# Optimization experiments

Hardware: AMD Instinct MI355X
Metric: run time of the kernel (lower is better)

## Reference

```python
import jax, jax.numpy as jnp
import numpy as np

N, H, n = 256, 64, 32
EPS = 1e-8  # eigenvalue floor for sqrt/rsqrt/log (SPD by construction, guard fp32)


def _sym_apply(X, fn, clip=True):
    """Apply scalar function fn to the eigenvalues of symmetric X (batched)."""
    w, V = jnp.linalg.eigh(X)
    if clip:
        w = jnp.clip(w, EPS)
    return jnp.einsum('...ij,...j,...kj->...ik', V, fn(w), V)


def _barygeom(Xf):
    """Riemannian barycenter via one Karcher-flow step (m_fun.BaryGeom, k=1).
    Xf: (M, n, n) SPD batch -> (n, n) Frechet mean."""
    G = jnp.mean(Xf, axis=0)                                   # arithmetic init
    G_sq = _sym_apply(G, jnp.sqrt)                             # G^{1/2}
    G_isq = _sym_apply(G, lambda w: 1.0 / jnp.sqrt(w))         # G^{-1/2}
    # mean of log(G^{-1/2} X G^{-1/2}) over the batch
    L = jnp.mean(_sym_apply(G_isq @ Xf @ G_isq, jnp.log), axis=0)
    expL = _sym_apply(L, jnp.exp, clip=False)                  # L symmetric, not PSD
    return G_sq @ expL @ G_sq


def setup_inputs() -> dict:
    key = jax.random.key(0)
    k1, k2 = jax.random.split(key)
    A = jax.random.normal(k1, (N, H, n, n), dtype=jnp.float32)
    # SPD inputs: A A^T / n + 0.1 I  -> well-conditioned covariance-like matrices
    X = jnp.einsum('bhij,bhkj->bhik', A, A) / n \
        + 0.1 * jnp.eye(n, dtype=jnp.float32)
    Bw = jax.random.normal(k2, (n, n), dtype=jnp.float32)
    weight = Bw @ Bw.T / n + 0.1 * jnp.eye(n, dtype=jnp.float32)  # SPD parameter
    return {"X": X, "weight": weight}


def reference(X, weight):
    Nb, Hc, nn_, _ = X.shape
    Xf = X.reshape(Nb * Hc, nn_, nn_)                 # (N*h, n, n), as in forward
    # Frechet mean is computed under torch.no_grad() in the original -> constant
    G = jax.lax.stop_gradient(_barygeom(Xf))
    G_isq = _sym_apply(G, lambda w: 1.0 / jnp.sqrt(w))
    Xc = G_isq @ Xf @ G_isq                           # CongrG(X, mean, 'neg')
    W_sq = _sym_apply(weight, jnp.sqrt)
    out = W_sq @ Xc @ W_sq                            # CongrG(Xc, weight, 'pos')
    return out.reshape(Nb, Hc, nn_, nn_)
```

## Files before the change

kernel.cpp:

```cpp
#include <hip/hip_runtime.h>
#include <math.h>

#define NMAT   16384
#define CHEB_A 0.08
#define CHEB_B 7.0
#define DDEG   29
#define NCOEF  (DDEG + 1)
#define NITER  ((DDEG - 1) / 2)
#define NLOGBLK 1024
#define NWAVES4 (NLOGBLK * 4)
#define NOUTBLK 1024
#define NOUTWV  (NOUTBLK * 4)

#define WS_GQ    0
#define WS_GSQ   1024
#define WS_C     2112
#define WS_CT    3136

#define OUT_PA   0
#define OUT_PL   262144
#define OUT_PL2  1310720

typedef __attribute__((ext_vector_type(8)))  short short8;
typedef __attribute__((ext_vector_type(16))) float f32x16;
typedef __attribute__((ext_vector_type(2)))  float f32x2;
typedef __attribute__((ext_vector_type(2)))  __bf16 bf16x2;

union FB { short8 v; unsigned int w[4]; };

#define ROWOF(r, h) (((r) & 3) + 8 * ((r) >> 2) + 4 * (h))

__device__ __forceinline__ unsigned int pk2(float a, float b) {
    unsigned int au = __float_as_uint(a) + 0x8000u;
    unsigned int bu = __float_as_uint(b) + 0x8000u;
    return __builtin_amdgcn_perm(bu, au, 0x07060302u);
}
__device__ __forceinline__ float rhi(float x) {
    return __uint_as_float((__float_as_uint(x) + 0x8000u) & 0xffff0000u);
}

__device__ __forceinline__ unsigned int cvt2(float a, float b) {
    f32x2 s; s.x = a; s.y = b;
    bf16x2 t = __builtin_convertvector(s, bf16x2);
    unsigned int r;
    __builtin_memcpy(&r, &t, 4);
    return r;
}

template <bool HALF>
__device__ __forceinline__ void toB(const f32x16& d, FB& b1, FB& b2) {
    unsigned int p[8];
#pragma unroll
    for (int g = 0; g < 8; ++g) {
        float s0 = HALF ? 0.5f * d[2 * g]     : d[2 * g];
        float s1 = HALF ? 0.5f * d[2 * g + 1] : d[2 * g + 1];
        p[g] = cvt2(s0, s1);
    }
    auto r02 = __builtin_amdgcn_permlane32_swap(p[0], p[2], false, false);
    auto r13 = __builtin_amdgcn_permlane32_swap(p[1], p[3], false, false);
    auto r46 = __builtin_amdgcn_permlane32_swap(p[4], p[6], false, false);
    auto r57 = __builtin_amdgcn_permlane32_swap(p[5], p[7], false, false);
    b1.w[0] = r02[0]; b1.w[1] = r13[0]; b1.w[2] = r02[1]; b1.w[3] = r13[1];
    b2.w[0] = r46[0]; b2.w[1] = r57[0]; b2.w[2] = r46[1]; b2.w[3] = r57[1];
}

#define MFMA(a, b, c) __builtin_amdgcn_mfma_f32_32x32x16_bf16((a), (b), (c), 0, 0, 0)

struct SplitM { FB h1, h2, l1, l2; };

__device__ __forceinline__ void splitB(const f32x16& d, SplitM& s) {
    unsigned int ph[8], pl[8];
#pragma unroll
    for (int g = 0; g < 8; ++g) {
        float a = d[2 * g], b = d[2 * g + 1];
        ph[g] = pk2(a, b);
        pl[g] = pk2(a - rhi(a), b - rhi(b));
    }
    auto h02 = __builtin_amdgcn_permlane32_swap(ph[0], ph[2], false, false);
    auto h13 = __builtin_amdgcn_permlane32_swap(ph[1], ph[3], false, false);
    auto h46 = __builtin_amdgcn_permlane32_swap(ph[4], ph[6], false, false);
    auto h57 = __builtin_amdgcn_permlane32_swap(ph[5], ph[7], false, false);
    s.h1.w[0] = h02[0]; s.h1.w[1] = h13[0]; s.h1.w[2] = h02[1]; s.h1.w[3] = h13[1];
    s.h2.w[0] = h46[0]; s.h2.w[1] = h57[0]; s.h2.w[2] = h46[1]; s.h2.w[3] = h57[1];
    auto l02 = __builtin_amdgcn_permlane32_swap(pl[0], pl[2], false, false);
    auto l13 = __builtin_amdgcn_permlane32_swap(pl[1], pl[3], false, false);
    auto l46 = __builtin_amdgcn_permlane32_swap(pl[4], pl[6], false, false);
    auto l57 = __builtin_amdgcn_permlane32_swap(pl[5], pl[7], false, false);
    s.l1.w[0] = l02[0]; s.l1.w[1] = l13[0]; s.l1.w[2] = l02[1]; s.l1.w[3] = l13[1];
    s.l2.w[0] = l46[0]; s.l2.w[1] = l57[0]; s.l2.w[2] = l46[1]; s.l2.w[3] = l57[1];
}

__device__ __forceinline__ f32x16 mulSS(const SplitM& A, const SplitM& B) {
    f32x16 d;
#pragma unroll
    for (int r = 0; r < 16; ++r) d[r] = 0.f;
    d = MFMA(A.h2.v, B.l2.v, d); d = MFMA(A.h1.v, B.l1.v, d);
    d = MFMA(A.l2.v, B.h2.v, d); d = MFMA(A.l1.v, B.h1.v, d);
    d = MFMA(A.h2.v, B.h2.v, d); d = MFMA(A.h1.v, B.h1.v, d);
    return d;
}

__device__ __forceinline__ void loadSplit(const float* __restrict__ base,
                                          int col, int h, SplitM& s) {
    const float* p = base + col * 32 + 8 * h;
    float4 a = *(const float4*)(p);
    float4 b = *(const float4*)(p + 4);
    float4 c = *(const float4*)(p + 16);
    float4 d = *(const float4*)(p + 20);
    s.h1.w[0] = pk2(a.x, a.y); s.h1.w[1] = pk2(a.z, a.w);
    s.h1.w[2] = pk2(b.x, b.y); s.h1.w[3] = pk2(b.z, b.w);
    s.h2.w[0] = pk2(c.x, c.y); s.h2.w[1] = pk2(c.z, c.w);
    s.h2.w[2] = pk2(d.x, d.y); s.h2.w[3] = pk2(d.z, d.w);
    s.l1.w[0] = pk2(a.x - rhi(a.x), a.y - rhi(a.y));
    s.l1.w[1] = pk2(a.z - rhi(a.z), a.w - rhi(a.w));
    s.l1.w[2] = pk2(b.x - rhi(b.x), b.y - rhi(b.y));
    s.l1.w[3] = pk2(b.z - rhi(b.z), b.w - rhi(b.w));
    s.l2.w[0] = pk2(c.x - rhi(c.x), c.y - rhi(c.y));
    s.l2.w[1] = pk2(c.z - rhi(c.z), c.w - rhi(c.w));
    s.l2.w[2] = pk2(d.x - rhi(d.x), d.y - rhi(d.y));
    s.l2.w[3] = pk2(d.z - rhi(d.z), d.w - rhi(d.w));
}

__device__ __forceinline__ float wred(float v) {
    v += __shfl_xor(v, 32);
    v += __shfl_xor(v, 16);
    v += __shfl_xor(v, 8);
    v += __shfl_xor(v, 4);
    v += __shfl_xor(v, 2);
    v += __shfl_xor(v, 1);
    return v;
}

__device__ __forceinline__ void mm32(const float* A, const float* B, float* D, int t) {
    int i = t >> 3, j0 = (t & 7) * 4;
    float a[32];
#pragma unroll
    for (int q = 0; q < 8; ++q) {
        float4 v = *(const float4*)&A[i * 32 + q * 4];
        a[4 * q] = v.x; a[4 * q + 1] = v.y; a[4 * q + 2] = v.z; a[4 * q + 3] = v.w;
    }
    float ax = 0.f, ay = 0.f, az = 0.f, aw = 0.f;
#pragma unroll
    for (int k = 0; k < 32; ++k) {
        float4 bv = *(const float4*)&B[k * 32 + j0];
        ax += a[k] * bv.x; ay += a[k] * bv.y; az += a[k] * bv.z; aw += a[k] * bv.w;
    }
    float4 r = { ax, ay, az, aw };
    *(float4*)&D[i * 32 + j0] = r;
}

__global__ __launch_bounds__(256) void k_psum(const float4* __restrict__ X4,
                                              float4* __restrict__ pA4) {
    int b = blockIdx.x, t = threadIdx.x;
    float4 acc = { 0.f, 0.f, 0.f, 0.f };
    for (int r = 0; r < 64; ++r) {
        float4 v = X4[(size_t)(b * 64 + r) * 256 + t];
        acc.x += v.x; acc.y += v.y; acc.z += v.z; acc.w += v.w;
    }
    pA4[b * 256 + t] = acc;
}

__global__ __launch_bounds__(256) void k_setup(const float4* __restrict__ pA4,
                                               float* __restrict__ ws) {
    __shared__ alignas(16) float sG[1024], sE[1024], sPa[1024], sPb[1024], sS1[1024], sS2[1024];
    __shared__ float sc[2];
    int t = threadIdx.x;
    float4 acc = { 0.f, 0.f, 0.f, 0.f };
    for (int b = 0; b < 256; ++b) {
        float4 v = pA4[b * 256 + t];
        acc.x += v.x; acc.y += v.y; acc.z += v.z; acc.w += v.w;
    }
    const float invM = 1.0f / (float)NMAT;
    sG[4 * t + 0] = acc.x * invM; sG[4 * t + 1] = acc.y * invM;
    sG[4 * t + 2] = acc.z * invM; sG[4 * t + 3] = acc.w * invM;
    __syncthreads();
    if (t == 0) { float s = 0.f; for (int d = 0; d < 32; ++d) s += sG[d * 33]; sc[0] = s / 32.0f; }
    __syncthreads();
    float c = sc[0];
    int i = t >> 3, j0 = (t & 7) * 4;
#pragma unroll
    for (int q = 0; q < 4; ++q) {
        int e = i * 32 + j0 + q;
        sE[e] = sG[e] / c - ((i == j0 + q) ? 1.f : 0.f);
    }
    __syncthreads();
    const float alp[9] = { 1.f, 0.5f, -0.125f, 0.0625f, -0.0390625f, 0.02734375f,
                           -0.0205078125f, 0.01611328125f, -0.013092041015625f };
    const float bet[9] = { 1.f, -0.5f, 0.375f, -0.3125f, 0.2734375f, -0.24609375f,
                           0.2255859375f, -0.20947265625f, 0.196380615234375f };
#pragma unroll
    for (int q = 0; q < 4; ++q) {
        int e = i * 32 + j0 + q;
        float d = (i == j0 + q) ? 1.f : 0.f;
        sS1[e] = d + alp[1] * sE[e];
        sS2[e] = d + bet[1] * sE[e];
        sPa[e] = sE[e];
    }
    __syncthreads();
    {
        float* P = sPa; float* Pn = sPb;
        for (int k = 2; k <= 8; ++k) {
            mm32(P, sE, Pn, t);
            __syncthreads();
#pragma unroll
            for (int q = 0; q < 4; ++q) {
                int e = i * 32 + j0 + q;
                sS1[e] += alp[k] * Pn[e];
                sS2[e] += bet[k] * Pn[e];
            }
            float* tmp = P; P = Pn; Pn = tmp;
            __syncthreads();
        }
    }
    float rc = sqrtf(c);
#pragma unroll
    for (int q = 0; q < 4; ++q) {
        int e = i * 32 + j0 + q;
        ws[WS_GSQ + e] = rc * sS1[e];
        ws[WS_GQ + e]  = sS2[e] / rc;
    }
}

__global__ __launch_bounds__(256, 2) void k_logsum(const float* __restrict__ Xg,
                                                   const float* __restrict__ ws,
                                                   float* __restrict__ pL) {
    __shared__ float sLacc[1024];
    __shared__ float scheb[NCOEF];
    int t = threadIdx.x;
    for (int e = t; e < 1024; e += 256) sLacc[e] = 0.f;
    if (t < NCOEF) {
        float alpha = 0.5f * (float)(CHEB_A + CHEB_B);
        float beta  = 0.5f * (float)(CHEB_B - CHEB_A);
        float dd = beta / alpha, s = sqrtf(1.f - dd * dd), tt = dd / (1.f + s);
        float v;
        if (t == 0) v = 2.f * (logf(alpha) + logf(0.5f * (1.f + s)));
        else        v = 2.f * ((t & 1) ? 1.f : -1.f) * exp2f((float)t * log2f(tt)) / (float)t;
        scheb[t] = v;
    }
    const int wv = t >> 6, lane = t & 63, h = lane >> 5, col = lane & 31;

    int hasd = (((col >> 2) & 1) == h);
    int dreg = 4 * (col >> 3) + (col & 3);
    f32x16 dm;
#pragma unroll
    for (int r = 0; r < 16; ++r) dm[r] = (hasd && r == dreg) ? 1.f : 0.f;

    FB GqH1, GqH2, GqL1, GqL2;
    {
        SplitM SGq;
        loadSplit(ws + WS_GQ, col, h, SGq);
        GqH1 = SGq.h1; GqH2 = SGq.h2; GqL1 = SGq.l1; GqL2 = SGq.l2;
    }
    __syncthreads();

    const float m2v = 2.0f / (float)(CHEB_B - CHEB_A);
    const float shv = (float)((CHEB_A + CHEB_B) / (CHEB_B - CHEB_A));
    const float tm = 2.f * m2v, tsh = -2.f * shv;
    const float cDv = scheb[DDEG], c0h = 0.5f * scheb[0];

    const int m0 = blockIdx.x * 4 + wv;

    const float* Xma = Xg + (size_t)(m0)                * 1024 + col * 32 + 8 * h;
    const float* Xmb = Xg + (size_t)(m0 + NWAVES4)      * 1024 + col * 32 + 8 * h;
    const float* Xmc = Xg + (size_t)(m0 + 2 * NWAVES4)  * 1024 + col * 32 + 8 * h;
    const float* Xmd = Xg + (size_t)(m0 + 3 * NWAVES4)  * 1024 + col * 32 + 8 * h;
    FB AXa1, AXa2, AXb1, AXb2, AXc1, AXc2, AXd1, AXd2;
    {
        float4 v0 = *(const float4*)(Xma);
        float4 v1 = *(const float4*)(Xma + 4);
        float4 v2 = *(const float4*)(Xma + 16);
        float4 v3 = *(const float4*)(Xma + 20);
        AXa1.w[0] = cvt2(v0.x, v0.y); AXa1.w[1] = cvt2(v0.z, v0.w);
        AXa1.w[2] = cvt2(v1.x, v1.y); AXa1.w[3] = cvt2(v1.z, v1.w);
        AXa2.w[0] = cvt2(v2.x, v2.y); AXa2.w[1] = cvt2(v2.z, v2.w);
        AXa2.w[2] = cvt2(v3.x, v3.y); AXa2.w[3] = cvt2(v3.z, v3.w);
    }
    {
        float4 v0 = *(const float4*)(Xmb);
        float4 v1 = *(const float4*)(Xmb + 4);
        float4 v2 = *(const float4*)(Xmb + 16);
        float4 v3 = *(const float4*)(Xmb + 20);
        AXb1.w[0] = cvt2(v0.x, v0.y); AXb1.w[1] = cvt2(v0.z, v0.w);
        AXb1.w[2] = cvt2(v1.x, v1.y); AXb1.w[3] = cvt2(v1.z, v1.w);
        AXb2.w[0] = cvt2(v2.x, v2.y); AXb2.w[1] = cvt2(v2.z, v2.w);
        AXb2.w[2] = cvt2(v3.x, v3.y); AXb2.w[3] = cvt2(v3.z, v3.w);
    }
    {
        float4 v0 = *(const float4*)(Xmc);
        float4 v1 = *(const float4*)(Xmc + 4);
        float4 v2 = *(const float4*)(Xmc + 16);
        float4 v3 = *(const float4*)(Xmc + 20);
        AXc1.w[0] = cvt2(v0.x, v0.y); AXc1.w[1] = cvt2(v0.z, v0.w);
        AXc1.w[2] = cvt2(v1.x, v1.y); AXc1.w[3] = cvt2(v1.z, v1.w);
        AXc2.w[0] = cvt2(v2.x, v2.y); AXc2.w[1] = cvt2(v2.z, v2.w);
        AXc2.w[2] = cvt2(v3.x, v3.y); AXc2.w[3] = cvt2(v3.z, v3.w);
    }
    {
        float4 v0 = *(const float4*)(Xmd);
        float4 v1 = *(const float4*)(Xmd + 4);
        float4 v2 = *(const float4*)(Xmd + 16);
        float4 v3 = *(const float4*)(Xmd + 20);
        AXd1.w[0] = cvt2(v0.x, v0.y); AXd1.w[1] = cvt2(v0.z, v0.w);
        AXd1.w[2] = cvt2(v1.x, v1.y); AXd1.w[3] = cvt2(v1.z, v1.w);
        AXd2.w[0] = cvt2(v2.x, v2.y); AXd2.w[1] = cvt2(v2.z, v2.w);
        AXd2.w[2] = cvt2(v3.x, v3.y); AXd2.w[3] = cvt2(v3.z, v3.w);
    }

    f32x16 Ua, Ub, Uc, Ud;
#pragma unroll
    for (int r = 0; r < 16; ++r) { Ua[r] = 0.f; Ub[r] = 0.f; Uc[r] = 0.f; Ud[r] = 0.f; }
    Ua = MFMA(AXa2.v, GqL2.v, Ua); Ub = MFMA(AXb2.v, GqL2.v, Ub);
    Uc = MFMA(AXc2.v, GqL2.v, Uc); Ud = MFMA(AXd2.v, GqL2.v, Ud);
    Ua = MFMA(AXa1.v, GqL1.v, Ua); Ub = MFMA(AXb1.v, GqL1.v, Ub);
    Uc = MFMA(AXc1.v, GqL1.v, Uc); Ud = MFMA(AXd1.v, GqL1.v, Ud);
    Ua = MFMA(AXa2.v, GqH2.v, Ua); Ub = MFMA(AXb2.v, GqH2.v, Ub);
    Uc = MFMA(AXc2.v, GqH2.v, Uc); Ud = MFMA(AXd2.v, GqH2.v, Ud);
    Ua = MFMA(AXa1.v, GqH1.v, Ua); Ub = MFMA(AXb1.v, GqH1.v, Ub);
    Uc = MFMA(AXc1.v, GqH1.v, Uc); Ud = MFMA(AXd1.v, GqH1.v, Ud);
    FB Ba1, Ba2, Bb1, Bb2, Bc1, Bc2, Bd1, Bd2;
    toB<false>(Ua, Ba1, Ba2); toB<false>(Ub, Bb1, Bb2);
    toB<false>(Uc, Bc1, Bc2); toB<false>(Ud, Bd1, Bd2);
    f32x16 Sa, Sb, Sc, Sd;
#pragma unroll
    for (int r = 0; r < 16; ++r) { Sa[r] = 0.f; Sb[r] = 0.f; Sc[r] = 0.f; Sd[r] = 0.f; }
    Sa = MFMA(GqL2.v, Ba2.v, Sa); Sb = MFMA(GqL2.v, Bb2.v, Sb);
    Sc = MFMA(GqL2.v, Bc2.v, Sc); Sd = MFMA(GqL2.v, Bd2.v, Sd);
    Sa = MFMA(GqL1.v, Ba1.v, Sa); Sb = MFMA(GqL1.v, Bb1.v, Sb);
    Sc = MFMA(GqL1.v, Bc1.v, Sc); Sd = MFMA(GqL1.v, Bd1.v, Sd);
    Sa = MFMA(GqH2.v, Ba2.v, Sa); Sb = MFMA(GqH2.v, Bb2.v, Sb);
    Sc = MFMA(GqH2.v, Bc2.v, Sc); Sd = MFMA(GqH2.v, Bd2.v, Sd);
    Sa = MFMA(GqH1.v, Ba1.v, Sa); Sb = MFMA(GqH1.v, Bb1.v, Sb);
    Sc = MFMA(GqH1.v, Bc1.v, Sc); Sd = MFMA(GqH1.v, Bd1.v, Sd);
    FB Aa1, Aa2, Ab1, Ab2, Ac1, Ac2, Ad1, Ad2;
    {
        f32x16 Ta, Tb, Tc, Td;
#pragma unroll
        for (int r = 0; r < 16; ++r) {
            Ta[r] = fmaf(tm, Sa[r], tsh * dm[r]);
            Tb[r] = fmaf(tm, Sb[r], tsh * dm[r]);
            Tc[r] = fmaf(tm, Sc[r], tsh * dm[r]);
            Td[r] = fmaf(tm, Sd[r], tsh * dm[r]);
        }
        toB<false>(Ta, Aa1, Aa2); toB<false>(Tb, Ab1, Ab2);
        toB<false>(Tc, Ac1, Ac2); toB<false>(Td, Ad1, Ad2);
    }

    f32x16 X0a, X1a, X0b, X1b, X0c, X1c, X0d, X1d;
#pragma unroll
    for (int r = 0; r < 16; ++r) {
        float cd = cDv * dm[r];
        X1a[r] = cd; X0a[r] = 0.f;
        X1b[r] = cd; X0b[r] = 0.f;
        X1c[r] = cd; X0c[r] = 0.f;
        X1d[r] = cd; X0d[r] = 0.f;
    }
    toB<false>(X1a, Ba1, Ba2);
    Bb1 = Ba1; Bb2 = Ba2; Bc1 = Ba1; Bc2 = Ba2; Bd1 = Ba1; Bd2 = Ba2;
    for (int it = 0; it < NITER; ++it) {
        float ka = scheb[DDEG - 1 - 2 * it];
        float kb = scheb[DDEG - 2 - 2 * it];
#pragma unroll
        for (int r = 0; r < 16; ++r) {
            float kd = ka * dm[r];
            X0a[r] = kd - X0a[r];
            X0b[r] = kd - X0b[r];
            X0c[r] = kd - X0c[r];
            X0d[r] = kd - X0d[r];
        }
        X0a = MFMA(Aa2.v, Ba2.v, X0a); X0b = MFMA(Ab2.v, Bb2.v, X0b);
        X0c = MFMA(Ac2.v, Bc2.v, X0c); X0d = MFMA(Ad2.v, Bd2.v, X0d);
        X0a = MFMA(Aa1.v, Ba1.v, X0a); X0b = MFMA(Ab1.v, Bb1.v, X0b);
        X0c = MFMA(Ac1.v, Bc1.v, X0c); X0d = MFMA(Ad1.v, Bd1.v, X0d);
        toB<false>(X0a, Ba1, Ba2); toB<false>(X0b, Bb1, Bb2);
        toB<false>(X0c, Bc1, Bc2); toB<false>(X0d, Bd1, Bd2);
#pragma unroll
        for (int r = 0; r < 16; ++r) {
            float kd = kb * dm[r];
            X1a[r] = kd - X1a[r];
            X1b[r] = kd - X1b[r];
            X1c[r] = kd - X1c[r];
            X1d[r] = kd - X1d[r];
        }
        X1a = MFMA(Aa2.v, Ba2.v, X1a); X1b = MFMA(Ab2.v, Bb2.v, X1b);
        X1c = MFMA(Ac2.v, Bc2.v, X1c); X1d = MFMA(Ad2.v, Bd2.v, X1d);
        X1a = MFMA(Aa1.v, Ba1.v, X1a); X1b = MFMA(Ab1.v, Bb1.v, X1b);
        X1c = MFMA(Ac1.v, Bc1.v, X1c); X1d = MFMA(Ad1.v, Bd1.v, X1d);
        if (it < NITER - 1) {
            toB<false>(X1a, Ba1, Ba2); toB<false>(X1b, Bb1, Bb2);
            toB<false>(X1c, Bc1, Bc2); toB<false>(X1d, Bd1, Bd2);
        } else {
            toB<true>(X1a, Ba1, Ba2); toB<true>(X1b, Bb1, Bb2);
            toB<true>(X1c, Bc1, Bc2); toB<true>(X1d, Bd1, Bd2);
        }
    }
#pragma unroll
    for (int r = 0; r < 16; ++r) {
        float kd = c0h * dm[r];
        X0a[r] = kd - X0a[r];
        X0b[r] = kd - X0b[r];
        X0c[r] = kd - X0c[r];
        X0d[r] = kd - X0d[r];
    }
    X0a = MFMA(Aa2.v, Ba2.v, X0a); X0b = MFMA(Ab2.v, Bb2.v, X0b);
    X0c = MFMA(Ac2.v, Bc2.v, X0c); X0d = MFMA(Ad2.v, Bd2.v, X0d);
    X0a = MFMA(Aa1.v, Ba1.v, X0a); X0b = MFMA(Ab1.v, Bb1.v, X0b);
    X0c = MFMA(Ac1.v, Bc1.v, X0c); X0d = MFMA(Ad1.v, Bd1.v, X0d);

    f32x16 Facc;
#pragma unroll
    for (int r = 0; r < 16; ++r) Facc[r] = (X0a[r] + X0b[r]) + (X0c[r] + X0d[r]);

#pragma unroll
    for (int r = 0; r < 16; ++r) {
        int row = (r & 3) + 8 * (r >> 2) + 4 * h;
        atomicAdd(&sLacc[row * 32 + col], Facc[r]);
    }
    __syncthreads();
    float4 v = *(float4*)&sLacc[4 * t];
    ((float4*)pL)[(size_t)blockIdx.x * 256 + t] = v;
}

__global__ __launch_bounds__(256) void k_red32(const float4* __restrict__ pL4,
                                               float4* __restrict__ pL24) {
    int b = blockIdx.x, t = threadIdx.x;
    float4 acc = { 0.f, 0.f, 0.f, 0.f };
    for (int r = 0; r < 32; ++r) {
        float4 v = pL4[(size_t)(b * 32 + r) * 256 + t];
        acc.x += v.x; acc.y += v.y; acc.z += v.z; acc.w += v.w;
    }
    pL24[b * 256 + t] = acc;
}

__global__ __launch_bounds__(256) void k_final(const float4* __restrict__ pL24,
                                               const float* __restrict__ Wg,
                                               float* __restrict__ ws) {
    __shared__ alignas(16) float sL[1024];
    int t = threadIdx.x;
    {
        float4 acc = { 0.f, 0.f, 0.f, 0.f };
        for (int b = 0; b < 32; ++b) {
            float4 v = pL24[b * 256 + t];
            acc.x += v.x; acc.y += v.y; acc.z += v.z; acc.w += v.w;
        }
        const float invM = 1.0f / (float)NMAT;
        sL[4 * t + 0] = acc.x * invM; sL[4 * t + 1] = acc.y * invM;
        sL[4 * t + 2] = acc.z * invM; sL[4 * t + 3] = acc.w * invM;
    }
    __syncthreads();
    if (t >= 64) return;

    const int h = t >> 5, col = t & 31;
    const int hasd = (((col >> 2) & 1) == h);
    const int dreg = 4 * (col >> 3) + (col & 3);
    f32x16 dm;
#pragma unroll
    for (int r = 0; r < 16; ++r) dm[r] = (hasd && r == dreg) ? 1.f : 0.f;

    f32x16 Lm;
#pragma unroll
    for (int r = 0; r < 16; ++r) Lm[r] = sL[ROWOF(r, h) * 32 + col];

    float tr = 0.f;
#pragma unroll
    for (int r = 0; r < 16; ++r) tr = fmaf(Lm[r], dm[r], tr);
    float s0 = wred(tr) / 32.0f;

    f32x16 L0;
#pragma unroll
    for (int r = 0; r < 16; ++r) L0[r] = fmaf(-s0, dm[r], Lm[r]);

    SplitM SL0; splitB(L0, SL0);
    f32x16 E4;
#pragma unroll
    for (int r = 0; r < 16; ++r) E4[r] = dm[r] + L0[r];
    SplitM SP = SL0;
    for (int k = 2; k <= 12; ++k) {
        f32x16 Pn = mulSS(SP, SL0);
        float invk = 1.0f / (float)k;
#pragma unroll
        for (int r = 0; r < 16; ++r) { Pn[r] *= invk; E4[r] += Pn[r]; }
        if (k < 12) splitB(Pn, SP);
    }
    float es = expf(s0);
#pragma unroll
    for (int r = 0; r < 16; ++r) E4[r] *= es;

    f32x16 Gs;
#pragma unroll
    for (int r = 0; r < 16; ++r) Gs[r] = ws[WS_GSQ + ROWOF(r, h) * 32 + col];
    SplitM SG; splitB(Gs, SG);
    SplitM SE; splitB(E4, SE);
    f32x16 Mx = mulSS(SE, SG);
    SplitM SM; splitB(Mx, SM);
    f32x16 Gn = mulSS(SG, SM);

    float tr2 = 0.f;
#pragma unroll
    for (int r = 0; r < 16; ++r) tr2 = fmaf(Gn[r], dm[r], tr2);
    float c2 = wred(tr2) / 32.0f;
    float ic2 = 1.0f / c2;

    f32x16 YC, ZC;
#pragma unroll
    for (int r = 0; r < 16; ++r) { YC[r] = Gn[r] * ic2; ZC[r] = dm[r]; }
    SplitM SY, SZ, ST;
    splitB(YC, SY); splitB(ZC, SZ);
    for (int it = 0; it < 8; ++it) {
        f32x16 ZY = mulSS(SZ, SY);
        f32x16 T;
#pragma unroll
        for (int r = 0; r < 16; ++r) T[r] = fmaf(1.5f, dm[r], -0.5f * ZY[r]);
        splitB(T, ST);
        f32x16 Yn = mulSS(SY, ST);
        f32x16 Zn = mulSS(ST, SZ);
        YC = Yn; ZC = Zn;
        splitB(YC, SY); splitB(ZC, SZ);
    }
    float rc2 = rsqrtf(c2);
    f32x16 Gi;
#pragma unroll
    for (int r = 0; r < 16; ++r) Gi[r] = ZC[r] * rc2;
    SplitM SGi; splitB(Gi, SGi);

    f32x16 Wm;
#pragma unroll
    for (int r = 0; r < 16; ++r) Wm[r] = Wg[ROWOF(r, h) * 32 + col];
    float ss = 0.f;
#pragma unroll
    for (int r = 0; r < 16; ++r) ss = fmaf(Wm[r], Wm[r], ss);
    float c3 = sqrtf(wred(ss));
    float ic3 = 1.0f / c3;
#pragma unroll
    for (int r = 0; r < 16; ++r) { YC[r] = Wm[r] * ic3; ZC[r] = dm[r]; }
    splitB(YC, SY); splitB(ZC, SZ);
    for (int it = 0; it < 15; ++it) {
        f32x16 ZY = mulSS(SZ, SY);
        f32x16 T;
#pragma unroll
        for (int r = 0; r < 16; ++r) T[r] = fmaf(1.5f, dm[r], -0.5f * ZY[r]);
        splitB(T, ST);
        f32x16 Yn = mulSS(SY, ST);
        f32x16 Zn = mulSS(ST, SZ);
        YC = Yn; ZC = Zn;
        splitB(YC, SY); splitB(ZC, SZ);
    }
    float rc3 = sqrtf(c3);
    f32x16 Ws;
#pragma unroll
    for (int r = 0; r < 16; ++r) Ws[r] = YC[r] * rc3;
    SplitM SW; splitB(Ws, SW);

    f32x16 C = mulSS(SW, SGi);
#pragma unroll
    for (int r = 0; r < 16; ++r) {
        int row = ROWOF(r, h);
        ws[WS_C + row * 32 + col] = C[r];
        ws[WS_CT + col * 32 + row] = C[r];
    }
}

__global__ __launch_bounds__(256) void k_out(const float* __restrict__ Xg,
                                             const float* __restrict__ ws,
                                             float* __restrict__ Og) {
    int t = threadIdx.x;
    const int wv = t >> 6, lane = t & 63, h = lane >> 5, col = lane & 31;
    SplitM SCt;
    loadSplit(ws + WS_C, col, h, SCt);

    for (int m = blockIdx.x * 4 + wv; m < NMAT; m += NOUTWV) {
        SplitM SX;
        loadSplit(Xg + (size_t)m * 1024, col, h, SX);
        f32x16 V = mulSS(SX, SCt);
        SplitM SV; splitB(V, SV);
        f32x16 O = mulSS(SCt, SV);
        float* Om = Og + (size_t)m * 1024;
#pragma unroll
        for (int r = 0; r < 16; ++r) {
            Om[ROWOF(r, h) * 32 + col] = O[r];
        }
    }
}

extern "C" void kernel_launch(void* const* d_in, const int* in_sizes, int n_in,
                              void* d_out, int out_size, void* d_ws, size_t ws_size,
                              hipStream_t stream) {
    const float* X = (const float*)d_in[0];
    const float* W = (const float*)d_in[1];
    float* out = (float*)d_out;
    float* ws  = (float*)d_ws;
    float* pA  = out + OUT_PA;
    float* pL  = out + OUT_PL;
    float* pL2 = out + OUT_PL2;

    hipLaunchKernelGGL(k_psum,   dim3(256),     dim3(256), 0, stream, (const float4*)X, (float4*)pA);
    hipLaunchKernelGGL(k_setup,  dim3(1),       dim3(256), 0, stream, (const float4*)pA, ws);
    hipLaunchKernelGGL(k_logsum, dim3(NLOGBLK), dim3(256), 0, stream, X, ws, pL);
    hipLaunchKernelGGL(k_red32,  dim3(32),      dim3(256), 0, stream, (const float4*)pL, (float4*)pL2);
    hipLaunchKernelGGL(k_final,  dim3(1),       dim3(256), 0, stream, (const float4*)pL2, W, ws);
    hipLaunchKernelGGL(k_out,    dim3(NOUTBLK), dim3(256), 0, stream, X, ws, out);
}
```

Baseline: 236.1 us.

## Inject Chebyshev diagonal terms via identity MFMAs instead of VALU loops

The Clenshaw recurrence in the log-sum kernel used to add diagonal coefficient terms and negate the accumulators with per-element VALU loops over a diagonal mask. These are now folded into extra MFMAs against bf16 identity fragments, using hi/lo split coefficients. The recurrence sign flips move into the bf16 conversion, and the affine scale is folded into the Gq factor as sqrt(tm). This takes VALU work off the critical path but adds 16 MFMAs per iteration step and changes rounding behaviour slightly.

```diff
diff --git a/kernel.cpp b/kernel.cpp
--- a/kernel.cpp
+++ b/kernel.cpp
@@ -47,13 +47,14 @@
     return r;
 }
 
-template <bool HALF>
+template <bool HALF, bool NEG>
 __device__ __forceinline__ void toB(const f32x16& d, FB& b1, FB& b2) {
     unsigned int p[8];
 #pragma unroll
     for (int g = 0; g < 8; ++g) {
-        float s0 = HALF ? 0.5f * d[2 * g]     : d[2 * g];
-        float s1 = HALF ? 0.5f * d[2 * g + 1] : d[2 * g + 1];
+        float s0 = d[2 * g], s1 = d[2 * g + 1];
+        if (HALF) { s0 *= 0.5f; s1 *= 0.5f; }
+        if (NEG)  { s0 = -s0; s1 = -s1; }
         p[g] = cvt2(s0, s1);
     }
     auto r02 = __builtin_amdgcn_permlane32_swap(p[0], p[2], false, false);
@@ -239,24 +240,72 @@
     }
     const int wv = t >> 6, lane = t & 63, h = lane >> 5, col = lane & 31;
 
-    int hasd = (((col >> 2) & 1) == h);
-    int dreg = 4 * (col >> 3) + (col & 3);
-    f32x16 dm;
-#pragma unroll
-    for (int r = 0; r < 16; ++r) dm[r] = (hasd && r == dreg) ? 1.f : 0.f;
-
-    FB GqH1, GqH2, GqL1, GqL2;
-    {
-        SplitM SGq;
-        loadSplit(ws + WS_GQ, col, h, SGq);
-        GqH1 = SGq.h1; GqH2 = SGq.h2; GqL1 = SGq.l1; GqL2 = SGq.l2;
-    }
-    __syncthreads();
+    const int inf1 = ((col >> 3) == h);
+    const int inf2 = ((col >> 3) == h + 2);
+    const int slot = col & 7;
+    const unsigned int hm = (slot & 1) ? 0xFFFF0000u : 0x0000FFFFu;
+    unsigned int mI1[4], mI2[4];
+#pragma unroll
+    for (int j = 0; j < 4; ++j) {
+        mI1[j] = (inf1 && (slot >> 1) == j) ? hm : 0u;
+        mI2[j] = (inf2 && (slot >> 1) == j) ? hm : 0u;
+    }
+    FB IA1, IA2;
+#pragma unroll
+    for (int j = 0; j < 4; ++j) {
+        IA1.w[j] = mI1[j] & 0x3F803F80u;
+        IA2.w[j] = mI2[j] & 0x3F803F80u;
+    }
 
     const float m2v = 2.0f / (float)(CHEB_B - CHEB_A);
     const float shv = (float)((CHEB_A + CHEB_B) / (CHEB_B - CHEB_A));
     const float tm = 2.f * m2v, tsh = -2.f * shv;
+    const float stm = sqrtf(tm);
+
+    FB GqH1, GqH2, GqL1, GqL2;
+    {
+        const float* Gqp = ws + WS_GQ + col * 32 + 8 * h;
+        float4 ga = *(const float4*)(Gqp);
+        float4 gb = *(const float4*)(Gqp + 4);
+        float4 gc = *(const float4*)(Gqp + 16);
+        float4 gd = *(const float4*)(Gqp + 20);
+        ga.x *= stm; ga.y *= stm; ga.z *= stm; ga.w *= stm;
+        gb.x *= stm; gb.y *= stm; gb.z *= stm; gb.w *= stm;
+        gc.x *= stm; gc.y *= stm; gc.z *= stm; gc.w *= stm;
+        gd.x *= stm; gd.y *= stm; gd.z *= stm; gd.w *= stm;
+        GqH1.w[0] = pk2(ga.x, ga.y); GqH1.w[1] = pk2(ga.z, ga.w);
+        GqH1.w[2] = pk2(gb.x, gb.y); GqH1.w[3] = pk2(gb.z, gb.w);
+        GqH2.w[0] = pk2(gc.x, gc.y); GqH2.w[1] = pk2(gc.z, gc.w);
+        GqH2.w[2] = pk2(gd.x, gd.y); GqH2.w[3] = pk2(gd.z, gd.w);
+        GqL1.w[0] = pk2(ga.x - rhi(ga.x), ga.y - rhi(ga.y));
+        GqL1.w[1] = pk2(ga.z - rhi(ga.z), ga.w - rhi(ga.w));
+        GqL1.w[2] = pk2(gb.x - rhi(gb.x), gb.y - rhi(gb.y));
+        GqL1.w[3] = pk2(gb.z - rhi(gb.z), gb.w - rhi(gb.w));
+        GqL2.w[0] = pk2(gc.x - rhi(gc.x), gc.y - rhi(gc.y));
+        GqL2.w[1] = pk2(gc.z - rhi(gc.z), gc.w - rhi(gc.w));
+        GqL2.w[2] = pk2(gd.x - rhi(gd.x), gd.y - rhi(gd.y));
+        GqL2.w[3] = pk2(gd.z - rhi(gd.z), gd.w - rhi(gd.w));
+    }
+    __syncthreads();
+
     const float cDv = scheb[DDEG], c0h = 0.5f * scheb[0];
+
+#define BUILD_KI(kf, v)                                                      \
+    {                                                                        \
+        float _v = (v);                                                      \
+        unsigned int _uh = cvt2(_v, _v);                                     \
+        float _vh = __uint_as_float(_uh & 0xFFFF0000u);                      \
+        float _vl = _v - _vh;                                                \
+        unsigned int _ul = cvt2(_vl, _vl);                                   \
+        _Pragma("unroll")                                                    \
+        for (int j = 0; j < 4; ++j) {                                        \
+            kf.h1.w[j] = mI1[j] & _uh; kf.h2.w[j] = mI2[j] & _uh;            \
+            kf.l1.w[j] = mI1[j] & _ul; kf.l2.w[j] = mI2[j] & _ul;            \
+        }                                                                    \
+    }
+#define ADD_KI(kf, acc)                                                      \
+    acc = MFMA(IA1.v, kf.h1.v, acc); acc = MFMA(IA2.v, kf.h2.v, acc);        \
+    acc = MFMA(IA1.v, kf.l1.v, acc); acc = MFMA(IA2.v, kf.l2.v, acc);
 
     const int m0 = blockIdx.x * 4 + wv;
 
@@ -318,11 +367,17 @@
     Ua = MFMA(AXa1.v, GqH1.v, Ua); Ub = MFMA(AXb1.v, GqH1.v, Ub);
     Uc = MFMA(AXc1.v, GqH1.v, Uc); Ud = MFMA(AXd1.v, GqH1.v, Ud);
     FB Ba1, Ba2, Bb1, Bb2, Bc1, Bc2, Bd1, Bd2;
-    toB<false>(Ua, Ba1, Ba2); toB<false>(Ub, Bb1, Bb2);
-    toB<false>(Uc, Bc1, Bc2); toB<false>(Ud, Bd1, Bd2);
-    f32x16 Sa, Sb, Sc, Sd;
-#pragma unroll
-    for (int r = 0; r < 16; ++r) { Sa[r] = 0.f; Sb[r] = 0.f; Sc[r] = 0.f; Sd[r] = 0.f; }
+    toB<false, false>(Ua, Ba1, Ba2); toB<false, false>(Ub, Bb1, Bb2);
+    toB<false, false>(Uc, Bc1, Bc2); toB<false, false>(Ud, Bd1, Bd2);
+
+    f32x16 Tseed;
+#pragma unroll
+    for (int r = 0; r < 16; ++r) Tseed[r] = 0.f;
+    {
+        SplitM kft; BUILD_KI(kft, tsh);
+        ADD_KI(kft, Tseed);
+    }
+    f32x16 Sa = Tseed, Sb = Tseed, Sc = Tseed, Sd = Tseed;
     Sa = MFMA(GqL2.v, Ba2.v, Sa); Sb = MFMA(GqL2.v, Bb2.v, Sb);
     Sc = MFMA(GqL2.v, Bc2.v, Sc); Sd = MFMA(GqL2.v, Bd2.v, Sd);
     Sa = MFMA(GqL1.v, Ba1.v, Sa); Sb = MFMA(GqL1.v, Bb1.v, Sb);
@@ -332,74 +387,61 @@
     Sa = MFMA(GqH1.v, Ba1.v, Sa); Sb = MFMA(GqH1.v, Bb1.v, Sb);
     Sc = MFMA(GqH1.v, Bc1.v, Sc); Sd = MFMA(GqH1.v, Bd1.v, Sd);
     FB Aa1, Aa2, Ab1, Ab2, Ac1, Ac2, Ad1, Ad2;
-    {
-        f32x16 Ta, Tb, Tc, Td;
-#pragma unroll
-        for (int r = 0; r < 16; ++r) {
-            Ta[r] = fmaf(tm, Sa[r], tsh * dm[r]);
-            Tb[r] = fmaf(tm, Sb[r], tsh * dm[r]);
-            Tc[r] = fmaf(tm, Sc[r], tsh * dm[r]);
-            Td[r] = fmaf(tm, Sd[r], tsh * dm[r]);
+    toB<false, false>(Sa, Aa1, Aa2); toB<false, false>(Sb, Ab1, Ab2);
+    toB<false, false>(Sc, Ac1, Ac2); toB<false, false>(Sd, Ad1, Ad2);
+
+    f32x16 X0a, X1a, X0b, X1b, X0c, X1c, X0d, X1d;
+    {
+        f32x16 X1s;
+#pragma unroll
+        for (int r = 0; r < 16; ++r) X1s[r] = 0.f;
+        SplitM kfs; BUILD_KI(kfs, -cDv);
+        ADD_KI(kfs, X1s);
+        X1a = X1s; X1b = X1s; X1c = X1s; X1d = X1s;
+#pragma unroll
+        for (int r = 0; r < 16; ++r) { X0a[r] = 0.f; X0b[r] = 0.f; X0c[r] = 0.f; X0d[r] = 0.f; }
+    }
+    {
+        unsigned int ucd = cvt2(cDv, cDv);
+#pragma unroll
+        for (int j = 0; j < 4; ++j) {
+            Ba1.w[j] = mI1[j] & ucd; Ba2.w[j] = mI2[j] & ucd;
         }
-        toB<false>(Ta, Aa1, Aa2); toB<false>(Tb, Ab1, Ab2);
-        toB<false>(Tc, Ac1, Ac2); toB<false>(Td, Ad1, Ad2);
-    }
-
-    f32x16 X0a, X1a, X0b, X1b, X0c, X1c, X0d, X1d;
-#pragma unroll
-    for (int r = 0; r < 16; ++r) {
-        float cd = cDv * dm[r];
-        X1a[r] = cd; X0a[r] = 0.f;
-        X1b[r] = cd; X0b[r] = 0.f;
-        X1c[r] = cd; X0c[r] = 0.f;
-        X1d[r] = cd; X0d[r] = 0.f;
-    }
-    toB<false>(X1a, Ba1, Ba2);
-    Bb1 = Ba1; Bb2 = Ba2; Bc1 = Ba1; Bc2 = Ba2; Bd1 = Ba1; Bd2 = Ba2;
+        Bb1 = Ba1; Bb2 = Ba2; Bc1 = Ba1; Bc2 = Ba2; Bd1 = Ba1; Bd2 = Ba2;
+    }
     for (int it = 0; it < NITER; ++it) {
-        float ka = scheb[DDEG - 1 - 2 * it];
-        float kb = scheb[DDEG - 2 - 2 * it];
-#pragma unroll
-        for (int r = 0; r < 16; ++r) {
-            float kd = ka * dm[r];
-            X0a[r] = kd - X0a[r];
-            X0b[r] = kd - X0b[r];
-            X0c[r] = kd - X0c[r];
-            X0d[r] = kd - X0d[r];
+        float sgn = (it & 1) ? -1.f : 1.f;
+        float ka = sgn * scheb[DDEG - 1 - 2 * it];
+        float kb = sgn * scheb[DDEG - 2 - 2 * it];
+        {
+            SplitM kfa; BUILD_KI(kfa, ka);
+            ADD_KI(kfa, X0a); ADD_KI(kfa, X0b); ADD_KI(kfa, X0c); ADD_KI(kfa, X0d);
         }
         X0a = MFMA(Aa2.v, Ba2.v, X0a); X0b = MFMA(Ab2.v, Bb2.v, X0b);
         X0c = MFMA(Ac2.v, Bc2.v, X0c); X0d = MFMA(Ad2.v, Bd2.v, X0d);
         X0a = MFMA(Aa1.v, Ba1.v, X0a); X0b = MFMA(Ab1.v, Bb1.v, X0b);
         X0c = MFMA(Ac1.v, Bc1.v, X0c); X0d = MFMA(Ad1.v, Bd1.v, X0d);
-        toB<false>(X0a, Ba1, Ba2); toB<false>(X0b, Bb1, Bb2);
-        toB<false>(X0c, Bc1, Bc2); toB<false>(X0d, Bd1, Bd2);
-#pragma unroll
-        for (int r = 0; r < 16; ++r) {
-            float kd = kb * dm[r];
-            X1a[r] = kd - X1a[r];
-            X1b[r] = kd - X1b[r];
-            X1c[r] = kd - X1c[r];
-            X1d[r] = kd - X1d[r];
+        toB<false, false>(X0a, Ba1, Ba2); toB<false, false>(X0b, Bb1, Bb2);
+        toB<false, false>(X0c, Bc1, Bc2); toB<false, false>(X0d, Bd1, Bd2);
+        {
+            SplitM kfb; BUILD_KI(kfb, kb);
+            ADD_KI(kfb, X1a); ADD_KI(kfb, X1b); ADD_KI(kfb, X1c); ADD_KI(kfb, X1d);
         }
         X1a = MFMA(Aa2.v, Ba2.v, X1a); X1b = MFMA(Ab2.v, Bb2.v, X1b);
         X1c = MFMA(Ac2.v, Bc2.v, X1c); X1d = MFMA(Ad2.v, Bd2.v, X1d);
         X1a = MFMA(Aa1.v, Ba1.v, X1a); X1b = MFMA(Ab1.v, Bb1.v, X1b);
         X1c = MFMA(Ac1.v, Bc1.v, X1c); X1d = MFMA(Ad1.v, Bd1.v, X1d);
         if (it < NITER - 1) {
-            toB<false>(X1a, Ba1, Ba2); toB<false>(X1b, Bb1, Bb2);
-            toB<false>(X1c, Bc1, Bc2); toB<false>(X1d, Bd1, Bd2);
+            toB<false, true>(X1a, Ba1, Ba2); toB<false, true>(X1b, Bb1, Bb2);
+            toB<false, true>(X1c, Bc1, Bc2); toB<false, true>(X1d, Bd1, Bd2);
         } else {
-            toB<true>(X1a, Ba1, Ba2); toB<true>(X1b, Bb1, Bb2);
-            toB<true>(X1c, Bc1, Bc2); toB<true>(X1d, Bd1, Bd2);
+            toB<true, true>(X1a, Ba1, Ba2); toB<true, true>(X1b, Bb1, Bb2);
+            toB<true, true>(X1c, Bc1, Bc2); toB<true, true>(X1d, Bd1, Bd2);
         }
     }
-#pragma unroll
-    for (int r = 0; r < 16; ++r) {
-        float kd = c0h * dm[r];
-        X0a[r] = kd - X0a[r];
-        X0b[r] = kd - X0b[r];
-        X0c[r] = kd - X0c[r];
-        X0d[r] = kd - X0d[r];
+    {
+        SplitM kf0; BUILD_KI(kf0, c0h);
+        ADD_KI(kf0, X0a); ADD_KI(kf0, X0b); ADD_KI(kf0, X0c); ADD_KI(kf0, X0d);
     }
     X0a = MFMA(Aa2.v, Ba2.v, X0a); X0b = MFMA(Ab2.v, Bb2.v, X0b);
     X0c = MFMA(Ac2.v, Bc2.v, X0c); X0d = MFMA(Ad2.v, Bd2.v, X0d);
@@ -418,6 +460,8 @@
     __syncthreads();
     float4 v = *(float4*)&sLacc[4 * t];
     ((float4*)pL)[(size_t)blockIdx.x * 256 + t] = v;
+#undef BUILD_KI
+#undef ADD_KI
 }
 
 __global__ __launch_bounds__(256) void k_red32(const float4* __restrict__ pL4,
```

Measured after the change: 253.4 us. 1.07x slower.

## Compute G^{1/2} and G^{-1/2} via MFMA Newton-Schulz iteration in setup kernel

Applied to the files above, without the earlier changes.

Replaces the 8-term binomial Taylor series for sqrt and inverse sqrt of the normalized mean, which used scalar LDS matrix multiplies, with a coupled Newton-Schulz (Denman-Beavers style) iteration. It runs on one 64-lane wave using split-precision MFMA products. The aim is to cut the serial latency of the single-block setup kernel and possibly improve accuracy. Seven of the eight waves now exit early, and the fixed 8 iterations with split matmuls add MFMA work and some convergence risk for poorly conditioned means.

```diff
diff --git a/kernel.cpp b/kernel.cpp
--- a/kernel.cpp
+++ b/kernel.cpp
@@ -131,24 +131,6 @@
     return v;
 }
 
-__device__ __forceinline__ void mm32(const float* A, const float* B, float* D, int t) {
-    int i = t >> 3, j0 = (t & 7) * 4;
-    float a[32];
-#pragma unroll
-    for (int q = 0; q < 8; ++q) {
-        float4 v = *(const float4*)&A[i * 32 + q * 4];
-        a[4 * q] = v.x; a[4 * q + 1] = v.y; a[4 * q + 2] = v.z; a[4 * q + 3] = v.w;
-    }
-    float ax = 0.f, ay = 0.f, az = 0.f, aw = 0.f;
-#pragma unroll
-    for (int k = 0; k < 32; ++k) {
-        float4 bv = *(const float4*)&B[k * 32 + j0];
-        ax += a[k] * bv.x; ay += a[k] * bv.y; az += a[k] * bv.z; aw += a[k] * bv.w;
-    }
-    float4 r = { ax, ay, az, aw };
-    *(float4*)&D[i * 32 + j0] = r;
-}
-
 __global__ __launch_bounds__(256) void k_psum(const float4* __restrict__ X4,
                                               float4* __restrict__ pA4) {
     int b = blockIdx.x, t = threadIdx.x;
@@ -162,62 +144,61 @@
 
 __global__ __launch_bounds__(256) void k_setup(const float4* __restrict__ pA4,
                                                float* __restrict__ ws) {
-    __shared__ alignas(16) float sG[1024], sE[1024], sPa[1024], sPb[1024], sS1[1024], sS2[1024];
-    __shared__ float sc[2];
+    __shared__ alignas(16) float sG[1024];
     int t = threadIdx.x;
-    float4 acc = { 0.f, 0.f, 0.f, 0.f };
-    for (int b = 0; b < 256; ++b) {
-        float4 v = pA4[b * 256 + t];
-        acc.x += v.x; acc.y += v.y; acc.z += v.z; acc.w += v.w;
-    }
-    const float invM = 1.0f / (float)NMAT;
-    sG[4 * t + 0] = acc.x * invM; sG[4 * t + 1] = acc.y * invM;
-    sG[4 * t + 2] = acc.z * invM; sG[4 * t + 3] = acc.w * invM;
+    {
+        float4 acc = { 0.f, 0.f, 0.f, 0.f };
+        for (int b = 0; b < 256; ++b) {
+            float4 v = pA4[b * 256 + t];
+            acc.x += v.x; acc.y += v.y; acc.z += v.z; acc.w += v.w;
+        }
+        const float invM = 1.0f / (float)NMAT;
+        sG[4 * t + 0] = acc.x * invM; sG[4 * t + 1] = acc.y * invM;
+        sG[4 * t + 2] = acc.z * invM; sG[4 * t + 3] = acc.w * invM;
+    }
     __syncthreads();
-    if (t == 0) { float s = 0.f; for (int d = 0; d < 32; ++d) s += sG[d * 33]; sc[0] = s / 32.0f; }
-    __syncthreads();
-    float c = sc[0];
-    int i = t >> 3, j0 = (t & 7) * 4;
-#pragma unroll
-    for (int q = 0; q < 4; ++q) {
-        int e = i * 32 + j0 + q;
-        sE[e] = sG[e] / c - ((i == j0 + q) ? 1.f : 0.f);
-    }
-    __syncthreads();
-    const float alp[9] = { 1.f, 0.5f, -0.125f, 0.0625f, -0.0390625f, 0.02734375f,
-                           -0.0205078125f, 0.01611328125f, -0.013092041015625f };
-    const float bet[9] = { 1.f, -0.5f, 0.375f, -0.3125f, 0.2734375f, -0.24609375f,
-                           0.2255859375f, -0.20947265625f, 0.196380615234375f };
-#pragma unroll
-    for (int q = 0; q < 4; ++q) {
-        int e = i * 32 + j0 + q;
-        float d = (i == j0 + q) ? 1.f : 0.f;
-        sS1[e] = d + alp[1] * sE[e];
-        sS2[e] = d + bet[1] * sE[e];
-        sPa[e] = sE[e];
-    }
-    __syncthreads();
-    {
-        float* P = sPa; float* Pn = sPb;
-        for (int k = 2; k <= 8; ++k) {
-            mm32(P, sE, Pn, t);
-            __syncthreads();
-#pragma unroll
-            for (int q = 0; q < 4; ++q) {
-                int e = i * 32 + j0 + q;
-                sS1[e] += alp[k] * Pn[e];
-                sS2[e] += bet[k] * Pn[e];
-            }
-            float* tmp = P; P = Pn; Pn = tmp;
-            __syncthreads();
-        }
+    if (t >= 64) return;
+
+    const int h = t >> 5, col = t & 31;
+    const int hasd = (((col >> 2) & 1) == h);
+    const int dreg = 4 * (col >> 3) + (col & 3);
+    f32x16 dm;
+#pragma unroll
+    for (int r = 0; r < 16; ++r) dm[r] = (hasd && r == dreg) ? 1.f : 0.f;
+
+    f32x16 Gm;
+#pragma unroll
+    for (int r = 0; r < 16; ++r) Gm[r] = sG[ROWOF(r, h) * 32 + col];
+
+    float tr = 0.f;
+#pragma unroll
+    for (int r = 0; r < 16; ++r) tr = fmaf(Gm[r], dm[r], tr);
+    float c = wred(tr) / 32.0f;
+    float ic = 1.0f / c;
+
+    f32x16 YC, ZC;
+#pragma unroll
+    for (int r = 0; r < 16; ++r) { YC[r] = Gm[r] * ic; ZC[r] = dm[r]; }
+    SplitM SY, SZ, ST;
+    splitB(YC, SY); splitB(ZC, SZ);
+    for (int it = 0; it < 8; ++it) {
+        f32x16 ZY = mulSS(SZ, SY);
+        f32x16 T;
+#pragma unroll
+        for (int r = 0; r < 16; ++r) T[r] = fmaf(1.5f, dm[r], -0.5f * ZY[r]);
+        splitB(T, ST);
+        f32x16 Yn = mulSS(SY, ST);
+        f32x16 Zn = mulSS(ST, SZ);
+        YC = Yn; ZC = Zn;
+        splitB(YC, SY); splitB(ZC, SZ);
     }
     float rc = sqrtf(c);
-#pragma unroll
-    for (int q = 0; q < 4; ++q) {
-        int e = i * 32 + j0 + q;
-        ws[WS_GSQ + e] = rc * sS1[e];
-        ws[WS_GQ + e]  = sS2[e] / rc;
+    float irc = 1.0f / rc;
+#pragma unroll
+    for (int r = 0; r < 16; ++r) {
+        int row = ROWOF(r, h);
+        ws[WS_GSQ + row * 32 + col] = YC[r] * rc;
+        ws[WS_GQ  + row * 32 + col] = ZC[r] * irc;
     }
 }
 
```

Measured after the change: 241.9 us, median of 2. 1.02x slower.
